# Optimization experiments

Hardware: AMD Instinct MI355X
Metric: run time of the kernel (lower is better)

Reference implementation:

```python
import jax, jax.numpy as jnp
import numpy as np

B, P, C = 64, 196, 768   # batch, num_patches, hidden_size
HS = 384                 # hidden_s (token-mixing hidden dim)
NG = 8                   # num_grids
GMIN, GMAX = -1.0, 1.0


def _rbf(x):
    # fast-KAN radial basis: exp(-((x - grid_i)/denom)^2), grid over [GMIN, GMAX]
    grid = jnp.linspace(GMIN, GMAX, NG).astype(x.dtype)
    denom = (GMAX - GMIN) / (NG - 1)
    return jnp.exp(-jnp.square((x[..., None] - grid) / denom))  # [..., din, NG]


def _kan_linear(x, spline_w, base_w, base_b):
    # x: [..., din]; spline_w: [dout, din*NG]; base_w: [dout, din]; base_b: [dout]
    basis = _rbf(x).reshape(*x.shape[:-1], -1)          # [..., din*NG]
    out = basis @ spline_w.T                            # spline term (no bias)
    out = out + jax.nn.silu(x) @ base_w.T + base_b      # base update term
    return out


def setup_inputs() -> dict:
    key = jax.random.key(0)
    ks = jax.random.split(key, 5)
    s = 0.1  # spline_weight_init_scale
    return {
        "x": jax.random.normal(ks[0], (B, P, C), jnp.float32),
        "fc1_spline_w": jax.random.normal(ks[1], (HS, P * NG), jnp.float32) * (s / np.sqrt(P * NG)),
        "fc1_base_w": jax.random.normal(ks[2], (HS, P), jnp.float32) / np.sqrt(P),
        "fc1_base_b": jnp.zeros((HS,), jnp.float32),
        "fc2_spline_w": jax.random.normal(ks[3], (P, HS * NG), jnp.float32) * (s / np.sqrt(HS * NG)),
        "fc2_base_w": jax.random.normal(ks[4], (P, HS), jnp.float32) / np.sqrt(HS),
        "fc2_base_b": jnp.zeros((P,), jnp.float32),
    }


def reference(x, fc1_spline_w, fc1_base_w, fc1_base_b,
              fc2_spline_w, fc2_base_w, fc2_base_b):
    skip_param = 1.0
    # token mixing: permute so KANLinear acts over the patch axis
    h = jnp.swapaxes(x, 1, 2)                                   # [B, C, P]
    h = _kan_linear(h, fc1_spline_w, fc1_base_w, fc1_base_b)    # [B, C, HS]
    # dropout p=0 -> identity; the two intermediate permutes cancel
    h = _kan_linear(h, fc2_spline_w, fc2_base_w, fc2_base_b)    # [B, C, P]
    out = jnp.swapaxes(h, 1, 2)                                 # [B, P, C]
    return out + skip_param * x
```

## Files before the change

kernel.cpp:

```cpp
#include <hip/hip_runtime.h>
#include <cstdint>

#define B_  64
#define P_  196
#define C_  768
#define HS_ 384
#define M_  49152

#define NC1 13
#define KT1 111
#define NT1 12
#define NC2 24
#define KT2 216
#define NT2 7

#define H1_ELEMS  ((size_t)M_ * HS_)
#define W1P_ELEMS ((size_t)KT1 * NT1 * 512)
#define W2P_ELEMS ((size_t)KT2 * NT2 * 512)

typedef __attribute__((ext_vector_type(8)))  short short8;
typedef __attribute__((ext_vector_type(16))) float f32x16;

#define MFMA(w, a, c) __builtin_amdgcn_mfma_f32_32x32x16_bf16((w), (a), (c), 0, 0, 0)

static __device__ __forceinline__ float bf2f(unsigned short u) {
    union { unsigned int i; float f; } v; v.i = ((unsigned int)u) << 16; return v.f;
}
static __device__ __forceinline__ unsigned short f2bf_rne(float f) {
    union { float f; unsigned int i; } v; v.f = f;
    unsigned int r = v.i + 0x7FFFu + ((v.i >> 16) & 1u);
    return (unsigned short)(r >> 16);
}
static __device__ __forceinline__ unsigned int pack2(float a, float b) {
    unsigned int ua = __float_as_uint(a) + 0x8000u;
    unsigned int ub = __float_as_uint(b) + 0x8000u;
    return __builtin_amdgcn_perm(ub, ua, 0x07060302u);
}
static __device__ __forceinline__ short8 rbf8(float s) {
    const float Rr = 1.2011224087864498f;
    const float Aa = 4.2039284307525743f;
    float t1 = __builtin_fmaf(Aa, s, Aa);
    union { short8 s8; unsigned int u[4]; } r;
#pragma unroll
    for (int q = 0; q < 4; q++) {
        float u0 = t1 - (float)(2 * q) * Rr;
        float u1 = t1 - (float)(2 * q + 1) * Rr;
        r.u[q] = pack2(__builtin_amdgcn_exp2f(-u0 * u0),
                       __builtin_amdgcn_exp2f(-u1 * u1));
    }
    return r.s8;
}
static __device__ __forceinline__ unsigned int silu2(float a, float b) {
    const float L2E = 1.4426950408889634f;
    float fa = a * __builtin_amdgcn_rcpf(1.f + __builtin_amdgcn_exp2f(-L2E * a));
    float fb = b * __builtin_amdgcn_rcpf(1.f + __builtin_amdgcn_exp2f(-L2E * b));
    return pack2(fa, fb);
}

__global__ void pack_w_kernel(const float* __restrict__ w1s,
                              const float* __restrict__ w1b,
                              const float* __restrict__ w2s,
                              const float* __restrict__ w2b,
                              unsigned short* __restrict__ w1p,
                              unsigned short* __restrict__ w2p) {
    size_t idx = (size_t)blockIdx.x * 256 + threadIdx.x;
    if (idx < W1P_ELEMS) {
        int j    = idx & 7;
        int lane = (idx >> 3) & 63;
        int lin  = idx >> 9;
        int nt   = lin % NT1;
        int tt   = lin / NT1;
        int cc   = (tt < 108) ? tt / 9 : 12;
        int kk   = (tt < 108) ? tt % 9 : (tt - 108);
        int ktl  = (cc < 12) ? kk : ((kk < 2) ? kk : 8);
        int n = nt * 32 + (lane & 31);
        int khalf = lane >> 5;
        float v = 0.f;
        if (ktl < 8) {
            int p = cc * 16 + ktl * 2 + khalf;
            if (p < P_) v = w1s[(size_t)n * 1568 + p * 8 + j];
        } else {
            int p = cc * 16 + khalf * 8 + j;
            if (p < P_) v = w1b[(size_t)n * 196 + p];
        }
        w1p[idx] = f2bf_rne(v);
    } else {
        size_t idx2 = idx - W1P_ELEMS;
        if (idx2 < W2P_ELEMS) {
            int j    = idx2 & 7;
            int lane = (idx2 >> 3) & 63;
            int lin  = idx2 >> 9;
            int nt   = lin % NT2;
            int tt   = lin / NT2;
            int cc   = tt / 9;
            int ktl  = tt % 9;
            int n = nt * 32 + (lane & 31);
            int khalf = lane >> 5;
            float v = 0.f;
            if (n < P_) {
                if (ktl < 8) {
                    int s = cc * 16 + ktl * 2 + khalf;
                    v = w2s[(size_t)n * 3072 + s * 8 + j];
                } else {
                    int s = cc * 16 + khalf * 8 + j;
                    v = w2b[(size_t)n * 384 + s];
                }
            }
            w2p[idx2] = f2bf_rne(v);
        }
    }
}

#define FB_  9216


__global__ __launch_bounds__(256, 2)
void fc1_kernel(const float* __restrict__ x,
                const unsigned short* __restrict__ w1p,
                const float* __restrict__ b1,
                unsigned short* __restrict__ h1t) {
    __shared__ __align__(16) unsigned short frag[2 * FB_];
    int blk = blockIdx.x;
    int tid = threadIdx.x;
    int b   = blk / 12;
    int c0  = (blk % 12) * 64;
    const float* xb = x + (size_t)b * (P_ * C_);

    int pr  = tid & 63;
    int sg  = tid >> 6;
    int prt = pr >> 5, pl31 = pr & 31;
    int pbase_rbf  = (prt << 9) + pl31 * 8;
    int pbase_silu = 8 * 1024 + (prt << 9) + (((sg >> 1) << 5) | pl31) * 8 + (sg & 1) * 4;

    int wave = sg, lane = tid & 63;
    int l31 = lane & 31, half = lane >> 5;
    int nt0 = wave * 3;

    f32x16 acc[2][3];
#pragma unroll
    for (int rt = 0; rt < 2; rt++)
#pragma unroll
        for (int nt = 0; nt < 3; nt++)
#pragma unroll
            for (int i = 0; i < 16; i++) acc[rt][nt][i] = 0.f;

    const short8* wp = (const short8*)w1p;
    short8 wbuf[3][3];

    auto wload = [&](int d, const short8* wt0, int kk) {
        const short8* wt = wt0 + (size_t)kk * (NT1 * 64);
        wbuf[d][0] = wt[0]; wbuf[d][1] = wt[64]; wbuf[d][2] = wt[128];
    };
    auto produce = [&](int fb, const float (&rb)[4]) {
#pragma unroll
        for (int i = 0; i < 4; i++) {
            int sl = sg * 4 + i;
            *(short8*)&frag[fb + (sl >> 1) * 1024 + ((sl & 1) << 8) + pbase_rbf] = rbf8(rb[i]);
        }
        uint2 sv;
        sv.x = silu2(rb[0], rb[1]);
        sv.y = silu2(rb[2], rb[3]);
        *(uint2*)&frag[fb + pbase_silu] = sv;
    };
    auto do_mfma = [&](short8 w0, short8 w1, short8 w2, short8 a0, short8 a1) {
        acc[0][0] = MFMA(w0, a0, acc[0][0]); acc[1][0] = MFMA(w0, a1, acc[1][0]);
        acc[0][1] = MFMA(w1, a0, acc[0][1]); acc[1][1] = MFMA(w1, a1, acc[1][1]);
        acc[0][2] = MFMA(w2, a0, acc[0][2]); acc[1][2] = MFMA(w2, a1, acc[1][2]);
    };
    auto body = [&](int cc, const float (&rbP)[4], float (&rbL)[4]) {
        const short8* wt0 = wp + ((size_t)(cc * 9) * NT1 + nt0) * 64 + lane;
        wload(0, wt0, 0); wload(1, wt0, 1); wload(2, wt0, 2);
        int fbP = ((cc + 1) & 1) * FB_;
        const unsigned short* fg = &frag[(cc & 1) * FB_];
        short8 a0 = *(const short8*)&fg[lane * 8];
        short8 a1 = *(const short8*)&fg[512 + lane * 8];
#pragma unroll
        for (int kk = 0; kk < 9; kk++) {
            short8 na0, na1;
            if (kk < 8) {
                na0 = *(const short8*)&fg[(kk + 1) * 1024 + lane * 8];
                na1 = *(const short8*)&fg[(kk + 1) * 1024 + 512 + lane * 8];
            }
            short8 w0 = wbuf[kk % 3][0], w1 = wbuf[kk % 3][1], w2 = wbuf[kk % 3][2];
            if (kk < 6) wload(kk % 3, wt0, kk + 3);
            if (kk < 4) {
                int sl = sg * 4 + kk;
                *(short8*)&frag[fbP + (sl >> 1) * 1024 + ((sl & 1) << 8) + pbase_rbf] = rbf8(rbP[kk]);
            } else if (kk == 4) {
                uint2 sv;
                sv.x = silu2(rbP[0], rbP[1]);
                sv.y = silu2(rbP[2], rbP[3]);
                *(uint2*)&frag[fbP + pbase_silu] = sv;
            } else {
                int i = kk - 5;
                int p = (cc + 2) * 16 + sg * 4 + i;
                p = (p < P_) ? p : (P_ - 1);
                rbL[i] = xb[(size_t)p * C_ + c0 + pr];
            }
            do_mfma(w0, w1, w2, a0, a1);
            if (kk < 8) { a0 = na0; a1 = na1; }
        }
        __syncthreads();
    };

    float rbA[4], rbB[4];
#pragma unroll
    for (int i = 0; i < 4; i++) {
        rbA[i] = xb[(size_t)(sg * 4 + i) * C_ + c0 + pr];
        rbB[i] = xb[(size_t)(16 + sg * 4 + i) * C_ + c0 + pr];
    }
    produce(0, rbA);
    __syncthreads();

    for (int c2 = 0; c2 < 6; c2++) {
        body(2 * c2,     rbB, rbA);
        body(2 * c2 + 1, rbA, rbB);
    }
    {
        const short8* wt0 = wp + ((size_t)108 * NT1 + nt0) * 64 + lane;
        wload(0, wt0, 0); wload(1, wt0, 1); wload(2, wt0, 2);
        const unsigned short* fg = &frag[0];
#pragma unroll
        for (int kk = 0; kk < 3; kk++) {
            int ktl = (kk < 2) ? kk : 8;
            short8 a0 = *(const short8*)&fg[ktl * 1024 + lane * 8];
            short8 a1 = *(const short8*)&fg[ktl * 1024 + 512 + lane * 8];
            do_mfma(wbuf[kk][0], wbuf[kk][1], wbuf[kk][2], a0, a1);
        }
    }

#pragma unroll
    for (int nt = 0; nt < 3; nt++) {
        int n0 = (nt0 + nt) * 32 + 4 * half;
#pragma unroll
        for (int reg = 0; reg < 16; reg++) {
            int n = n0 + (reg & 3) + 8 * (reg >> 2);
            float bv = b1[n];
#pragma unroll
            for (int rt = 0; rt < 2; rt++) {
                h1t[(size_t)n * M_ + blk * 64 + rt * 32 + l31] = f2bf_rne(acc[rt][nt][reg] + bv);
            }
        }
    }
}

__global__ __launch_bounds__(256, 2)
void fc2_kernel(const unsigned short* __restrict__ h1t,
                const unsigned short* __restrict__ w2p,
                const float* __restrict__ b2,
                const float* __restrict__ x,
                float* __restrict__ out) {
    __shared__ __align__(16) unsigned short frag[2 * FB_];
    int blk = blockIdx.x;
    int tid = threadIdx.x;
    int rbase = blk * 64;

    int pr  = tid & 63;
    int sg  = tid >> 6;
    int prt = pr >> 5, pl31 = pr & 31;
    int pbase_rbf  = (prt << 9) + pl31 * 8;
    int pbase_silu = 8 * 1024 + (prt << 9) + (((sg >> 1) << 5) | pl31) * 8 + (sg & 1) * 4;

    int wave = sg, lane = tid & 63;
    int l31 = lane & 31, half = lane >> 5;
    int nt0 = wave * 2;
    int ntn = (wave < 3) ? 2 : 1;
    int off1 = (ntn > 1) ? 64 : 0;

    f32x16 acc[2][2];
#pragma unroll
    for (int rt = 0; rt < 2; rt++)
#pragma unroll
        for (int nt = 0; nt < 2; nt++)
#pragma unroll
            for (int i = 0; i < 16; i++) acc[rt][nt][i] = 0.f;

    const short8* wp = (const short8*)w2p;
    short8 wbuf[3][2];

    auto wload = [&](int d, const short8* wt0, int kk) {
        const short8* wt = wt0 + (size_t)kk * (NT2 * 64);
        wbuf[d][0] = wt[0]; wbuf[d][1] = wt[off1];
    };
    auto produce = [&](int fb, const unsigned short (&rb)[4]) {
        float v0 = bf2f(rb[0]), v1 = bf2f(rb[1]), v2 = bf2f(rb[2]), v3 = bf2f(rb[3]);
        float vv[4] = {v0, v1, v2, v3};
#pragma unroll
        for (int i = 0; i < 4; i++) {
            int sl = sg * 4 + i;
            *(short8*)&frag[fb + (sl >> 1) * 1024 + ((sl & 1) << 8) + pbase_rbf] = rbf8(vv[i]);
        }
        uint2 sv;
        sv.x = silu2(v0, v1);
        sv.y = silu2(v2, v3);
        *(uint2*)&frag[fb + pbase_silu] = sv;
    };
    auto do_mfma = [&](short8 w0, short8 w1, short8 a0, short8 a1) {
        acc[0][0] = MFMA(w0, a0, acc[0][0]); acc[1][0] = MFMA(w0, a1, acc[1][0]);
        if (ntn == 2) {
            acc[0][1] = MFMA(w1, a0, acc[0][1]); acc[1][1] = MFMA(w1, a1, acc[1][1]);
        }
    };
    auto body = [&](int cc, const unsigned short (&rbP)[4], unsigned short (&rbL)[4]) {
        bool doProd = (cc + 1 < NC2);
        const short8* wt0 = wp + ((size_t)(cc * 9) * NT2 + nt0) * 64 + lane;
        wload(0, wt0, 0); wload(1, wt0, 1); wload(2, wt0, 2);
        int fbP = ((cc + 1) & 1) * FB_;
        const unsigned short* fg = &frag[(cc & 1) * FB_];
        short8 a0 = *(const short8*)&fg[lane * 8];
        short8 a1 = *(const short8*)&fg[512 + lane * 8];
#pragma unroll
        for (int kk = 0; kk < 9; kk++) {
            short8 na0, na1;
            if (kk < 8) {
                na0 = *(const short8*)&fg[(kk + 1) * 1024 + lane * 8];
                na1 = *(const short8*)&fg[(kk + 1) * 1024 + 512 + lane * 8];
            }
            short8 w0 = wbuf[kk % 3][0], w1 = wbuf[kk % 3][1];
            if (kk < 6) wload(kk % 3, wt0, kk + 3);
            if (kk < 4) {
                if (doProd) {
                    int sl = sg * 4 + kk;
                    *(short8*)&frag[fbP + (sl >> 1) * 1024 + ((sl & 1) << 8) + pbase_rbf] =
                        rbf8(bf2f(rbP[kk]));
                }
            } else if (kk == 4) {
                if (doProd) {
                    uint2 sv;
                    sv.x = silu2(bf2f(rbP[0]), bf2f(rbP[1]));
                    sv.y = silu2(bf2f(rbP[2]), bf2f(rbP[3]));
                    *(uint2*)&frag[fbP + pbase_silu] = sv;
                }
            } else {
                int i = kk - 5;
                int s = (cc + 2) * 16 + sg * 4 + i;
                s = (s < HS_) ? s : (HS_ - 1);
                rbL[i] = h1t[(size_t)s * M_ + rbase + pr];
            }
            do_mfma(w0, w1, a0, a1);
            if (kk < 8) { a0 = na0; a1 = na1; }
        }
        __syncthreads();
    };

    unsigned short rbA[4], rbB[4];
#pragma unroll
    for (int i = 0; i < 4; i++) {
        rbA[i] = h1t[(size_t)(sg * 4 + i) * M_ + rbase + pr];
        rbB[i] = h1t[(size_t)(16 + sg * 4 + i) * M_ + rbase + pr];
    }
    produce(0, rbA);
    __syncthreads();

    for (int c2 = 0; c2 < 12; c2++) {
        body(2 * c2,     rbB, rbA);
        body(2 * c2 + 1, rbA, rbB);
    }

    int b = blk / 12;
    int c0 = (blk % 12) * 64;
#pragma unroll
    for (int nt = 0; nt < 2; nt++) {
        if (nt < ntn) {
            int p0 = (nt0 + nt) * 32 + 4 * half;
#pragma unroll
            for (int reg = 0; reg < 16; reg++) {
                int p = p0 + (reg & 3) + 8 * (reg >> 2);
                if (p < P_) {
                    float bv = b2[p];
#pragma unroll
                    for (int rt = 0; rt < 2; rt++) {
                        size_t off = ((size_t)b * P_ + p) * C_ + c0 + rt * 32 + l31;
                        out[off] = acc[rt][nt][reg] + bv + x[off];
                    }
                }
            }
        }
    }
}

extern "C" void kernel_launch(void* const* d_in, const int* in_sizes, int n_in,
                              void* d_out, int out_size, void* d_ws, size_t ws_size,
                              hipStream_t stream) {
    const float* x   = (const float*)d_in[0];
    const float* w1s = (const float*)d_in[1];
    const float* w1b = (const float*)d_in[2];
    const float* b1  = (const float*)d_in[3];
    const float* w2s = (const float*)d_in[4];
    const float* w2b = (const float*)d_in[5];
    const float* b2  = (const float*)d_in[6];
    float* out = (float*)d_out;

    unsigned short* h1t = (unsigned short*)d_ws;
    unsigned short* w1p = h1t + H1_ELEMS;
    unsigned short* w2p = w1p + W1P_ELEMS;

    int pack_blocks = (int)((W1P_ELEMS + W2P_ELEMS) / 256);
    pack_w_kernel<<<pack_blocks, 256, 0, stream>>>(w1s, w1b, w2s, w2b, w1p, w2p);
    fc1_kernel<<<M_ / 64, 256, 0, stream>>>(x, w1p, b1, h1t);
    fc2_kernel<<<M_ / 64, 256, 0, stream>>>(h1t, w2p, b2, x, out);
}
```

Measured before the change: 278.7 us.

## Enlarge row tile from 64 to 96 rows per block in both KAN GEMM kernels

Each block now handles 96 rows (three 32-row MFMA tiles) instead of 64 in both fc1 and fc2. Every weight fragment loaded from global memory is therefore reused across more rows, and the grid shrinks from 768 to 512 blocks. The RBF/SiLU producer is split into two thread groups to cover the extra 32 columns, the LDS tile stride grows to 1536, and the weight register prefetch depth drops from 3 to 2 stages to offset the extra accumulator registers. The trade-offs are higher register and LDS use, which may lower occupancy or cause spills under launch_bounds(256,2), fewer blocks to spread across CUs, and a shallower weight prefetch that may expose load latency.

```diff
diff --git a/kernel.cpp b/kernel.cpp
--- a/kernel.cpp
+++ b/kernel.cpp
@@ -6,6 +6,8 @@
 #define C_  768
 #define HS_ 384
 #define M_  49152
+#define RT_ 96
+#define NB_ (M_ / RT_)
 
 #define NC1 13
 #define KT1 111
@@ -111,7 +113,8 @@
     }
 }
 
-#define FB_  9216
+#define TS_  1536
+#define FB_  (9 * TS_)
 
 
 __global__ __launch_bounds__(256, 2)
@@ -122,110 +125,152 @@
     __shared__ __align__(16) unsigned short frag[2 * FB_];
     int blk = blockIdx.x;
     int tid = threadIdx.x;
-    int b   = blk / 12;
-    int c0  = (blk % 12) * 64;
+    int b   = blk >> 3;
+    int c0  = (blk & 7) * RT_;
     const float* xb = x + (size_t)b * (P_ * C_);
 
-    int pr  = tid & 63;
-    int sg  = tid >> 6;
-    int prt = pr >> 5, pl31 = pr & 31;
-    int pbase_rbf  = (prt << 9) + pl31 * 8;
-    int pbase_silu = 8 * 1024 + (prt << 9) + (((sg >> 1) << 5) | pl31) * 8 + (sg & 1) * 4;
-
-    int wave = sg, lane = tid & 63;
+    int colA = tid & 63, scA = tid >> 6;
+    int colB = 64 + (tid & 31), scB = tid >> 5;
+    int pbase_rbfA  = ((colA >> 5) << 9) + (colA & 31) * 8;
+    int pbase_rbfB  = 1024 + (colB & 31) * 8;
+    int pbase_siluA = 8 * TS_ + ((colA >> 5) << 9) + ((scA >> 1) << 8) + (colA & 31) * 8 + (scA & 1) * 4;
+    int pbase_siluB = 8 * TS_ + 1024 + ((scB >> 2) << 8) + (colB & 31) * 8 + (scB & 3) * 2;
+
+    int wave = tid >> 6, lane = tid & 63;
     int l31 = lane & 31, half = lane >> 5;
     int nt0 = wave * 3;
 
-    f32x16 acc[2][3];
-#pragma unroll
-    for (int rt = 0; rt < 2; rt++)
+    f32x16 acc[3][3];
+#pragma unroll
+    for (int rt = 0; rt < 3; rt++)
 #pragma unroll
         for (int nt = 0; nt < 3; nt++)
 #pragma unroll
             for (int i = 0; i < 16; i++) acc[rt][nt][i] = 0.f;
 
     const short8* wp = (const short8*)w1p;
-    short8 wbuf[3][3];
+    short8 wbuf[2][3];
 
     auto wload = [&](int d, const short8* wt0, int kk) {
         const short8* wt = wt0 + (size_t)kk * (NT1 * 64);
         wbuf[d][0] = wt[0]; wbuf[d][1] = wt[64]; wbuf[d][2] = wt[128];
     };
-    auto produce = [&](int fb, const float (&rb)[4]) {
+    auto do_mfma = [&](short8 w0, short8 w1, short8 w2,
+                       short8 a0, short8 a1, short8 a2) {
+        acc[0][0] = MFMA(w0, a0, acc[0][0]); acc[1][0] = MFMA(w0, a1, acc[1][0]); acc[2][0] = MFMA(w0, a2, acc[2][0]);
+        acc[0][1] = MFMA(w1, a0, acc[0][1]); acc[1][1] = MFMA(w1, a1, acc[1][1]); acc[2][1] = MFMA(w1, a2, acc[2][1]);
+        acc[0][2] = MFMA(w2, a0, acc[0][2]); acc[1][2] = MFMA(w2, a1, acc[1][2]); acc[2][2] = MFMA(w2, a2, acc[2][2]);
+    };
+    auto produce = [&](int fb, const float (&ra)[4], const float (&rb2)[2]) {
 #pragma unroll
         for (int i = 0; i < 4; i++) {
-            int sl = sg * 4 + i;
-            *(short8*)&frag[fb + (sl >> 1) * 1024 + ((sl & 1) << 8) + pbase_rbf] = rbf8(rb[i]);
+            int sl = scA * 4 + i;
+            *(short8*)&frag[fb + (sl >> 1) * TS_ + ((sl & 1) << 8) + pbase_rbfA] = rbf8(ra[i]);
+        }
+#pragma unroll
+        for (int i = 0; i < 2; i++) {
+            int sl = scB * 2 + i;
+            *(short8*)&frag[fb + (sl >> 1) * TS_ + ((sl & 1) << 8) + pbase_rbfB] = rbf8(rb2[i]);
         }
         uint2 sv;
-        sv.x = silu2(rb[0], rb[1]);
-        sv.y = silu2(rb[2], rb[3]);
-        *(uint2*)&frag[fb + pbase_silu] = sv;
-    };
-    auto do_mfma = [&](short8 w0, short8 w1, short8 w2, short8 a0, short8 a1) {
-        acc[0][0] = MFMA(w0, a0, acc[0][0]); acc[1][0] = MFMA(w0, a1, acc[1][0]);
-        acc[0][1] = MFMA(w1, a0, acc[0][1]); acc[1][1] = MFMA(w1, a1, acc[1][1]);
-        acc[0][2] = MFMA(w2, a0, acc[0][2]); acc[1][2] = MFMA(w2, a1, acc[1][2]);
-    };
-    auto body = [&](int cc, const float (&rbP)[4], float (&rbL)[4]) {
+        sv.x = silu2(ra[0], ra[1]);
+        sv.y = silu2(ra[2], ra[3]);
+        *(uint2*)&frag[fb + pbase_siluA] = sv;
+        *(unsigned int*)&frag[fb + pbase_siluB] = silu2(rb2[0], rb2[1]);
+    };
+    auto body = [&](int cc, const float (&rbPA)[4], const float (&rbPB)[2],
+                    float (&rbLA)[4], float (&rbLB)[2]) {
         const short8* wt0 = wp + ((size_t)(cc * 9) * NT1 + nt0) * 64 + lane;
-        wload(0, wt0, 0); wload(1, wt0, 1); wload(2, wt0, 2);
+        wload(0, wt0, 0); wload(1, wt0, 1);
         int fbP = ((cc + 1) & 1) * FB_;
         const unsigned short* fg = &frag[(cc & 1) * FB_];
         short8 a0 = *(const short8*)&fg[lane * 8];
         short8 a1 = *(const short8*)&fg[512 + lane * 8];
+        short8 a2 = *(const short8*)&fg[1024 + lane * 8];
 #pragma unroll
         for (int kk = 0; kk < 9; kk++) {
-            short8 na0, na1;
+            short8 na0, na1, na2;
             if (kk < 8) {
-                na0 = *(const short8*)&fg[(kk + 1) * 1024 + lane * 8];
-                na1 = *(const short8*)&fg[(kk + 1) * 1024 + 512 + lane * 8];
-            }
-            short8 w0 = wbuf[kk % 3][0], w1 = wbuf[kk % 3][1], w2 = wbuf[kk % 3][2];
-            if (kk < 6) wload(kk % 3, wt0, kk + 3);
+                na0 = *(const short8*)&fg[(kk + 1) * TS_ + lane * 8];
+                na1 = *(const short8*)&fg[(kk + 1) * TS_ + 512 + lane * 8];
+                na2 = *(const short8*)&fg[(kk + 1) * TS_ + 1024 + lane * 8];
+            }
+            short8 w0 = wbuf[kk & 1][0], w1 = wbuf[kk & 1][1], w2 = wbuf[kk & 1][2];
+            if (kk < 7) wload(kk & 1, wt0, kk + 2);
             if (kk < 4) {
-                int sl = sg * 4 + kk;
-                *(short8*)&frag[fbP + (sl >> 1) * 1024 + ((sl & 1) << 8) + pbase_rbf] = rbf8(rbP[kk]);
+                int sl = scA * 4 + kk;
+                *(short8*)&frag[fbP + (sl >> 1) * TS_ + ((sl & 1) << 8) + pbase_rbfA] = rbf8(rbPA[kk]);
             } else if (kk == 4) {
+#pragma unroll
+                for (int i = 0; i < 2; i++) {
+                    int sl = scB * 2 + i;
+                    *(short8*)&frag[fbP + (sl >> 1) * TS_ + ((sl & 1) << 8) + pbase_rbfB] = rbf8(rbPB[i]);
+                }
+            } else if (kk == 5) {
                 uint2 sv;
-                sv.x = silu2(rbP[0], rbP[1]);
-                sv.y = silu2(rbP[2], rbP[3]);
-                *(uint2*)&frag[fbP + pbase_silu] = sv;
+                sv.x = silu2(rbPA[0], rbPA[1]);
+                sv.y = silu2(rbPA[2], rbPA[3]);
+                *(uint2*)&frag[fbP + pbase_siluA] = sv;
+                *(unsigned int*)&frag[fbP + pbase_siluB] = silu2(rbPB[0], rbPB[1]);
+            } else if (kk == 6) {
+#pragma unroll
+                for (int i = 0; i < 2; i++) {
+                    int p = (cc + 2) * 16 + scA * 4 + i;
+                    p = (p < P_) ? p : (P_ - 1);
+                    rbLA[i] = xb[(size_t)p * C_ + c0 + colA];
+                }
+            } else if (kk == 7) {
+#pragma unroll
+                for (int i = 2; i < 4; i++) {
+                    int p = (cc + 2) * 16 + scA * 4 + i;
+                    p = (p < P_) ? p : (P_ - 1);
+                    rbLA[i] = xb[(size_t)p * C_ + c0 + colA];
+                }
             } else {
-                int i = kk - 5;
-                int p = (cc + 2) * 16 + sg * 4 + i;
-                p = (p < P_) ? p : (P_ - 1);
-                rbL[i] = xb[(size_t)p * C_ + c0 + pr];
-            }
-            do_mfma(w0, w1, w2, a0, a1);
-            if (kk < 8) { a0 = na0; a1 = na1; }
+#pragma unroll
+                for (int i = 0; i < 2; i++) {
+                    int p = (cc + 2) * 16 + scB * 2 + i;
+                    p = (p < P_) ? p : (P_ - 1);
+                    rbLB[i] = xb[(size_t)p * C_ + c0 + colB];
+                }
+            }
+            do_mfma(w0, w1, w2, a0, a1, a2);
+            if (kk < 8) { a0 = na0; a1 = na1; a2 = na2; }
         }
         __syncthreads();
     };
 
-    float rbA[4], rbB[4];
+    float rbA_A[4], rbB_A[4], rbA_B[2], rbB_B[2];
 #pragma unroll
     for (int i = 0; i < 4; i++) {
-        rbA[i] = xb[(size_t)(sg * 4 + i) * C_ + c0 + pr];
-        rbB[i] = xb[(size_t)(16 + sg * 4 + i) * C_ + c0 + pr];
-    }
-    produce(0, rbA);
+        rbA_A[i] = xb[(size_t)(scA * 4 + i) * C_ + c0 + colA];
+        rbB_A[i] = xb[(size_t)(16 + scA * 4 + i) * C_ + c0 + colA];
+    }
+#pragma unroll
+    for (int i = 0; i < 2; i++) {
+        rbA_B[i] = xb[(size_t)(scB * 2 + i) * C_ + c0 + colB];
+        rbB_B[i] = xb[(size_t)(16 + scB * 2 + i) * C_ + c0 + colB];
+    }
+    produce(0, rbA_A, rbA_B);
     __syncthreads();
 
     for (int c2 = 0; c2 < 6; c2++) {
-        body(2 * c2,     rbB, rbA);
-        body(2 * c2 + 1, rbA, rbB);
+        body(2 * c2,     rbB_A, rbB_B, rbA_A, rbA_B);
+        body(2 * c2 + 1, rbA_A, rbA_B, rbB_A, rbB_B);
     }
     {
         const short8* wt0 = wp + ((size_t)108 * NT1 + nt0) * 64 + lane;
-        wload(0, wt0, 0); wload(1, wt0, 1); wload(2, wt0, 2);
+        wload(0, wt0, 0); wload(1, wt0, 1);
         const unsigned short* fg = &frag[0];
 #pragma unroll
         for (int kk = 0; kk < 3; kk++) {
+            short8 w0 = wbuf[kk & 1][0], w1 = wbuf[kk & 1][1], w2 = wbuf[kk & 1][2];
+            if (kk == 0) wload(0, wt0, 2);
             int ktl = (kk < 2) ? kk : 8;
-            short8 a0 = *(const short8*)&fg[ktl * 1024 + lane * 8];
-            short8 a1 = *(const short8*)&fg[ktl * 1024 + 512 + lane * 8];
-            do_mfma(wbuf[kk][0], wbuf[kk][1], wbuf[kk][2], a0, a1);
+            short8 a0 = *(const short8*)&fg[ktl * TS_ + lane * 8];
+            short8 a1 = *(const short8*)&fg[ktl * TS_ + 512 + lane * 8];
+            short8 a2 = *(const short8*)&fg[ktl * TS_ + 1024 + lane * 8];
+            do_mfma(w0, w1, w2, a0, a1, a2);
         }
     }
 
@@ -237,8 +282,8 @@
             int n = n0 + (reg & 3) + 8 * (reg >> 2);
             float bv = b1[n];
 #pragma unroll
-            for (int rt = 0; rt < 2; rt++) {
-                h1t[(size_t)n * M_ + blk * 64 + rt * 32 + l31] = f2bf_rne(acc[rt][nt][reg] + bv);
+            for (int rt = 0; rt < 3; rt++) {
+                h1t[(size_t)n * M_ + blk * RT_ + rt * 32 + l31] = f2bf_rne(acc[rt][nt][reg] + bv);
             }
         }
     }
@@ -253,112 +298,155 @@
     __shared__ __align__(16) unsigned short frag[2 * FB_];
     int blk = blockIdx.x;
     int tid = threadIdx.x;
-    int rbase = blk * 64;
-
-    int pr  = tid & 63;
-    int sg  = tid >> 6;
-    int prt = pr >> 5, pl31 = pr & 31;
-    int pbase_rbf  = (prt << 9) + pl31 * 8;
-    int pbase_silu = 8 * 1024 + (prt << 9) + (((sg >> 1) << 5) | pl31) * 8 + (sg & 1) * 4;
-
-    int wave = sg, lane = tid & 63;
+    int rbase = blk * RT_;
+
+    int colA = tid & 63, scA = tid >> 6;
+    int colB = 64 + (tid & 31), scB = tid >> 5;
+    int pbase_rbfA  = ((colA >> 5) << 9) + (colA & 31) * 8;
+    int pbase_rbfB  = 1024 + (colB & 31) * 8;
+    int pbase_siluA = 8 * TS_ + ((colA >> 5) << 9) + ((scA >> 1) << 8) + (colA & 31) * 8 + (scA & 1) * 4;
+    int pbase_siluB = 8 * TS_ + 1024 + ((scB >> 2) << 8) + (colB & 31) * 8 + (scB & 3) * 2;
+
+    int wave = tid >> 6, lane = tid & 63;
     int l31 = lane & 31, half = lane >> 5;
     int nt0 = wave * 2;
     int ntn = (wave < 3) ? 2 : 1;
     int off1 = (ntn > 1) ? 64 : 0;
 
-    f32x16 acc[2][2];
-#pragma unroll
-    for (int rt = 0; rt < 2; rt++)
+    f32x16 acc[3][2];
+#pragma unroll
+    for (int rt = 0; rt < 3; rt++)
 #pragma unroll
         for (int nt = 0; nt < 2; nt++)
 #pragma unroll
             for (int i = 0; i < 16; i++) acc[rt][nt][i] = 0.f;
 
     const short8* wp = (const short8*)w2p;
-    short8 wbuf[3][2];
+    short8 wbuf[2][2];
 
     auto wload = [&](int d, const short8* wt0, int kk) {
         const short8* wt = wt0 + (size_t)kk * (NT2 * 64);
         wbuf[d][0] = wt[0]; wbuf[d][1] = wt[off1];
     };
-    auto produce = [&](int fb, const unsigned short (&rb)[4]) {
-        float v0 = bf2f(rb[0]), v1 = bf2f(rb[1]), v2 = bf2f(rb[2]), v3 = bf2f(rb[3]);
+    auto do_mfma = [&](short8 w0, short8 w1, short8 a0, short8 a1, short8 a2) {
+        acc[0][0] = MFMA(w0, a0, acc[0][0]); acc[1][0] = MFMA(w0, a1, acc[1][0]); acc[2][0] = MFMA(w0, a2, acc[2][0]);
+        if (ntn == 2) {
+            acc[0][1] = MFMA(w1, a0, acc[0][1]); acc[1][1] = MFMA(w1, a1, acc[1][1]); acc[2][1] = MFMA(w1, a2, acc[2][1]);
+        }
+    };
+    auto produce = [&](int fb, const unsigned short (&ra)[4], const unsigned short (&rb2)[2]) {
+        float v0 = bf2f(ra[0]), v1 = bf2f(ra[1]), v2 = bf2f(ra[2]), v3 = bf2f(ra[3]);
+        float u0 = bf2f(rb2[0]), u1 = bf2f(rb2[1]);
         float vv[4] = {v0, v1, v2, v3};
 #pragma unroll
         for (int i = 0; i < 4; i++) {
-            int sl = sg * 4 + i;
-            *(short8*)&frag[fb + (sl >> 1) * 1024 + ((sl & 1) << 8) + pbase_rbf] = rbf8(vv[i]);
+            int sl = scA * 4 + i;
+            *(short8*)&frag[fb + (sl >> 1) * TS_ + ((sl & 1) << 8) + pbase_rbfA] = rbf8(vv[i]);
+        }
+        float uu[2] = {u0, u1};
+#pragma unroll
+        for (int i = 0; i < 2; i++) {
+            int sl = scB * 2 + i;
+            *(short8*)&frag[fb + (sl >> 1) * TS_ + ((sl & 1) << 8) + pbase_rbfB] = rbf8(uu[i]);
         }
         uint2 sv;
         sv.x = silu2(v0, v1);
         sv.y = silu2(v2, v3);
-        *(uint2*)&frag[fb + pbase_silu] = sv;
-    };
-    auto do_mfma = [&](short8 w0, short8 w1, short8 a0, short8 a1) {
-        acc[0][0] = MFMA(w0, a0, acc[0][0]); acc[1][0] = MFMA(w0, a1, acc[1][0]);
-        if (ntn == 2) {
-            acc[0][1] = MFMA(w1, a0, acc[0][1]); acc[1][1] = MFMA(w1, a1, acc[1][1]);
-        }
-    };
-    auto body = [&](int cc, const unsigned short (&rbP)[4], unsigned short (&rbL)[4]) {
+        *(uint2*)&frag[fb + pbase_siluA] = sv;
+        *(unsigned int*)&frag[fb + pbase_siluB] = silu2(u0, u1);
+    };
+    auto body = [&](int cc, const unsigned short (&rbPA)[4], const unsigned short (&rbPB)[2],
+                    unsigned short (&rbLA)[4], unsigned short (&rbLB)[2]) {
         bool doProd = (cc + 1 < NC2);
         const short8* wt0 = wp + ((size_t)(cc * 9) * NT2 + nt0) * 64 + lane;
-        wload(0, wt0, 0); wload(1, wt0, 1); wload(2, wt0, 2);
+        wload(0, wt0, 0); wload(1, wt0, 1);
         int fbP = ((cc + 1) & 1) * FB_;
         const unsigned short* fg = &frag[(cc & 1) * FB_];
         short8 a0 = *(const short8*)&fg[lane * 8];
         short8 a1 = *(const short8*)&fg[512 + lane * 8];
+        short8 a2 = *(const short8*)&fg[1024 + lane * 8];
 #pragma unroll
         for (int kk = 0; kk < 9; kk++) {
-            short8 na0, na1;
+            short8 na0, na1, na2;
             if (kk < 8) {
-                na0 = *(const short8*)&fg[(kk + 1) * 1024 + lane * 8];
-                na1 = *(const short8*)&fg[(kk + 1) * 1024 + 512 + lane * 8];
-            }
-            short8 w0 = wbuf[kk % 3][0], w1 = wbuf[kk % 3][1];
-            if (kk < 6) wload(kk % 3, wt0, kk + 3);
+                na0 = *(const short8*)&fg[(kk + 1) * TS_ + lane * 8];
+                na1 = *(const short8*)&fg[(kk + 1) * TS_ + 512 + lane * 8];
+                na2 = *(const short8*)&fg[(kk + 1) * TS_ + 1024 + lane * 8];
+            }
+            short8 w0 = wbuf[kk & 1][0], w1 = wbuf[kk & 1][1];
+            if (kk < 7) wload(kk & 1, wt0, kk + 2);
             if (kk < 4) {
                 if (doProd) {
-                    int sl = sg * 4 + kk;
-                    *(short8*)&frag[fbP + (sl >> 1) * 1024 + ((sl & 1) << 8) + pbase_rbf] =
-                        rbf8(bf2f(rbP[kk]));
+                    int sl = scA * 4 + kk;
+                    *(short8*)&frag[fbP + (sl >> 1) * TS_ + ((sl & 1) << 8) + pbase_rbfA] =
+                        rbf8(bf2f(rbPA[kk]));
                 }
             } else if (kk == 4) {
                 if (doProd) {
+#pragma unroll
+                    for (int i = 0; i < 2; i++) {
+                        int sl = scB * 2 + i;
+                        *(short8*)&frag[fbP + (sl >> 1) * TS_ + ((sl & 1) << 8) + pbase_rbfB] =
+                            rbf8(bf2f(rbPB[i]));
+                    }
+                }
+            } else if (kk == 5) {
+                if (doProd) {
                     uint2 sv;
-                    sv.x = silu2(bf2f(rbP[0]), bf2f(rbP[1]));
-                    sv.y = silu2(bf2f(rbP[2]), bf2f(rbP[3]));
-                    *(uint2*)&frag[fbP + pbase_silu] = sv;
+                    sv.x = silu2(bf2f(rbPA[0]), bf2f(rbPA[1]));
+                    sv.y = silu2(bf2f(rbPA[2]), bf2f(rbPA[3]));
+                    *(uint2*)&frag[fbP + pbase_siluA] = sv;
+                    *(unsigned int*)&frag[fbP + pbase_siluB] = silu2(bf2f(rbPB[0]), bf2f(rbPB[1]));
+                }
+            } else if (kk == 6) {
+#pragma unroll
+                for (int i = 0; i < 2; i++) {
+                    int s = (cc + 2) * 16 + scA * 4 + i;
+                    s = (s < HS_) ? s : (HS_ - 1);
+                    rbLA[i] = h1t[(size_t)s * M_ + rbase + colA];
+                }
+            } else if (kk == 7) {
+#pragma unroll
+                for (int i = 2; i < 4; i++) {
+                    int s = (cc + 2) * 16 + scA * 4 + i;
+                    s = (s < HS_) ? s : (HS_ - 1);
+                    rbLA[i] = h1t[(size_t)s * M_ + rbase + colA];
                 }
             } else {
-                int i = kk - 5;
-                int s = (cc + 2) * 16 + sg * 4 + i;
-                s = (s < HS_) ? s : (HS_ - 1);
-                rbL[i] = h1t[(size_t)s * M_ + rbase + pr];
-            }
-            do_mfma(w0, w1, a0, a1);
-            if (kk < 8) { a0 = na0; a1 = na1; }
+#pragma unroll
+                for (int i = 0; i < 2; i++) {
+                    int s = (cc + 2) * 16 + scB * 2 + i;
+                    s = (s < HS_) ? s : (HS_ - 1);
+                    rbLB[i] = h1t[(size_t)s * M_ + rbase + colB];
+                }
+            }
+            do_mfma(w0, w1, a0, a1, a2);
+            if (kk < 8) { a0 = na0; a1 = na1; a2 = na2; }
         }
         __syncthreads();
     };
 
-    unsigned short rbA[4], rbB[4];
+    unsigned short rbA_A[4], rbB_A[4], rbA_B[2], rbB_B[2];
 #pragma unroll
     for (int i = 0; i < 4; i++) {
-        rbA[i] = h1t[(size_t)(sg * 4 + i) * M_ + rbase + pr];
-        rbB[i] = h1t[(size_t)(16 + sg * 4 + i) * M_ + rbase + pr];
-    }
-    produce(0, rbA);
+        rbA_A[i] = h1t[(size_t)(scA * 4 + i) * M_ + rbase + colA];
+        rbB_A[i] = h1t[(size_t)(16 + scA * 4 + i) * M_ + rbase + colA];
+    }
+#pragma unroll
+    for (int i = 0; i < 2; i++) {
+        rbA_B[i] = h1t[(size_t)(scB * 2 + i) * M_ + rbase + colB];
+        rbB_B[i] = h1t[(size_t)(16 + scB * 2 + i) * M_ + rbase + colB];
+    }
+    produce(0, rbA_A, rbA_B);
     __syncthreads();
 
     for (int c2 = 0; c2 < 12; c2++) {
-        body(2 * c2,     rbB, rbA);
-        body(2 * c2 + 1, rbA, rbB);
-    }
-
-    int b = blk / 12;
-    int c0 = (blk % 12) * 64;
+        body(2 * c2,     rbB_A, rbB_B, rbA_A, rbA_B);
+        body(2 * c2 + 1, rbA_A, rbA_B, rbB_A, rbB_B);
+    }
+
+    int b = blk >> 3;
+    int c0 = (blk & 7) * RT_;
 #pragma unroll
     for (int nt = 0; nt < 2; nt++) {
         if (nt < ntn) {
@@ -369,7 +457,7 @@
                 if (p < P_) {
                     float bv = b2[p];
 #pragma unroll
-                    for (int rt = 0; rt < 2; rt++) {
+                    for (int rt = 0; rt < 3; rt++) {
                         size_t off = ((size_t)b * P_ + p) * C_ + c0 + rt * 32 + l31;
                         out[off] = acc[rt][nt][reg] + bv + x[off];
                     }
@@ -397,6 +485,6 @@
 
     int pack_blocks = (int)((W1P_ELEMS + W2P_ELEMS) / 256);
     pack_w_kernel<<<pack_blocks, 256, 0, stream>>>(w1s, w1b, w2s, w2b, w1p, w2p);
-    fc1_kernel<<<M_ / 64, 256, 0, stream>>>(x, w1p, b1, h1t);
-    fc2_kernel<<<M_ / 64, 256, 0, stream>>>(h1t, w2p, b2, x, out);
-}
+    fc1_kernel<<<NB_, 256, 0, stream>>>(x, w1p, b1, h1t);
+    fc2_kernel<<<NB_, 256, 0, stream>>>(h1t, w2p, b2, x, out);
+}
```

Measured after the change: 248.5 us. 10.8% less time.
